# Kernel tuning notes

Hardware: AMD Instinct MI355X
Metric: run time of the kernel (lower is better)

## Reference

```python
import jax, jax.numpy as jnp
import numpy as np

B, S, E = 8, 1024, 512
H = 8            # num_heads
D = E // H       # head_dim
FFN = 2048
WINDOW = 5       # local_window_size
EPS = 1e-5


def _mha(x, in_w, in_b, out_w, out_b, mask=None):
    """PyTorch nn.MultiheadAttention (batch_first) forward. mask: True = blocked."""
    b, s, e = x.shape
    qkv = x @ in_w.T + in_b                      # [B,S,3E]
    q, k, v = jnp.split(qkv, 3, axis=-1)
    def heads(t):
        return t.reshape(b, s, H, D).transpose(0, 2, 1, 3)  # [B,H,S,D]
    q, k, v = heads(q), heads(k), heads(v)
    scores = jnp.einsum('bhsd,bhtd->bhst', q, k) / np.sqrt(D).astype(x.dtype)
    if mask is not None:
        scores = jnp.where(mask[None, None], -jnp.inf, scores)
    attn = jax.nn.softmax(scores, axis=-1)
    out = jnp.einsum('bhst,bhtd->bhsd', attn, v)  # [B,H,S,D]
    out = out.transpose(0, 2, 1, 3).reshape(b, s, e)
    return out @ out_w.T + out_b


def _layernorm(x, g, b):
    mu = jnp.mean(x, axis=-1, keepdims=True)
    var = jnp.mean(jnp.square(x - mu), axis=-1, keepdims=True)
    return (x - mu) * jax.lax.rsqrt(var + EPS) * g + b


def setup_inputs() -> dict:
    key = jax.random.key(0)
    ks = jax.random.split(key, 8)
    w = 0.02  # weight scale for numerical sanity
    return {
        'x': jax.random.normal(ks[0], (B, S, E), jnp.float32),
        'l_in_w': jax.random.normal(ks[1], (3 * E, E), jnp.float32) * w,
        'l_in_b': jnp.zeros((3 * E,), jnp.float32),
        'l_out_w': jax.random.normal(ks[2], (E, E), jnp.float32) * w,
        'l_out_b': jnp.zeros((E,), jnp.float32),
        'g_in_w': jax.random.normal(ks[3], (3 * E, E), jnp.float32) * w,
        'g_in_b': jnp.zeros((3 * E,), jnp.float32),
        'g_out_w': jax.random.normal(ks[4], (E, E), jnp.float32) * w,
        'g_out_b': jnp.zeros((E,), jnp.float32),
        'ffn_w1': jax.random.normal(ks[5], (FFN, E), jnp.float32) * w,
        'ffn_b1': jnp.zeros((FFN,), jnp.float32),
        'ffn_w2': jax.random.normal(ks[6], (E, FFN), jnp.float32) * w,
        'ffn_b2': jnp.zeros((E,), jnp.float32),
        'ln1_g': jnp.ones((E,), jnp.float32),
        'ln1_b': jnp.zeros((E,), jnp.float32),
        'ln2_g': jnp.ones((E,), jnp.float32),
        'ln2_b': jnp.zeros((E,), jnp.float32),
    }


def reference(x, l_in_w, l_in_b, l_out_w, l_out_b,
              g_in_w, g_in_b, g_out_w, g_out_b,
              ffn_w1, ffn_b1, ffn_w2, ffn_b2,
              ln1_g, ln1_b, ln2_g, ln2_b):
    s = x.shape[1]
    idx = jnp.arange(s)
    local_mask = jnp.abs(idx[:, None] - idx[None, :]) > WINDOW  # True = blocked
    local_out = _mha(x, l_in_w, l_in_b, l_out_w, l_out_b, mask=local_mask)
    global_out = _mha(x, g_in_w, g_in_b, g_out_w, g_out_b)
    x = x + local_out + global_out
    x = _layernorm(x, ln1_g, ln1_b)
    ffn = jax.nn.relu(x @ ffn_w1.T + ffn_b1) @ ffn_w2.T + ffn_b2
    x = _layernorm(x + ffn, ln2_g, ln2_b)
    return x
```

## Files before the change

kernel.cpp:

```cpp
#include <hip/hip_runtime.h>
#include <hip/hip_bf16.h>
#include <stdint.h>

#define Bb 8
#define Ss 1024
#define Ee 512
#define Hh 8
#define Dh 64
#define FFNd 2048
#define EPSv 1e-5f
#define QS 3072

typedef float f32x4 __attribute__((ext_vector_type(4)));
typedef int   i32x4 __attribute__((ext_vector_type(4)));

__device__ inline float bf2f(ushort u) {
    uint32_t x = ((uint32_t)u) << 16; float f; __builtin_memcpy(&f, &x, 4); return f;
}
__device__ inline ushort f2bf(float f) {
    uint32_t x; __builtin_memcpy(&x, &f, 4);
    uint32_t r = (x + 0x7FFFu + ((x >> 16) & 1u)) >> 16; return (ushort)r;
}

__device__ inline void gload16(const ushort* g, ushort* l) {
    __builtin_amdgcn_global_load_lds((const __attribute__((address_space(1))) void*)g,
                                     (__attribute__((address_space(3))) void*)l,
                                     16, 0, 0);
}

__device__ inline int vswz(int d, int kv) {
    return (d * 64 + kv) ^ ((((d & 7) ^ ((d >> 3) & 7)) & 7) << 3);
}

__global__ __launch_bounds__(256) void cvt_all(const float* __restrict__ s0, const float* __restrict__ s1,
                                               const float* __restrict__ s2, const float* __restrict__ s3,
                                               const float* __restrict__ s4, const float* __restrict__ s5,
                                               const float* __restrict__ s6,
                                               ushort* __restrict__ dx, ushort* __restrict__ dw) {
    int bid = blockIdx.x;
    const float* src; ushort* dst; int boff;
    if (bid < 4096)      { src = s0; dst = dx;            boff = bid; }
    else if (bid < 4864) { src = s1; dst = dw;            boff = bid - 4096; }
    else if (bid < 5632) { src = s2; dst = dw + 786432;   boff = bid - 4864; }
    else if (bid < 5888) { src = s3; dst = dw + 1572864;  boff = bid - 5632; }
    else if (bid < 6144) { src = s4; dst = dw + 1835008;  boff = bid - 5888; }
    else if (bid < 7168) { src = s5; dst = dw + 2097152;  boff = bid - 6144; }
    else                 { src = s6; dst = dw + 3145728;  boff = bid - 7168; }
    int i = boff * 256 + threadIdx.x;
    float4 v = ((const float4*)src)[i];
    ushort4 o;
    o.x = f2bf(v.x); o.y = f2bf(v.y); o.z = f2bf(v.z); o.w = f2bf(v.w);
    ((ushort4*)dst)[i] = o;
}

template<bool OUT_BF16, bool RELU>
__global__ __launch_bounds__(256) void gemm_bt(const ushort* __restrict__ A,
                                               const ushort* __restrict__ Bm,
                                               const float* __restrict__ bias,
                                               const float* __restrict__ bias2, int nb1,
                                               void* __restrict__ C,
                                               int M, int N, int K) {
    __shared__ ushort Alds[128 * 32];
    __shared__ ushort Blds[128 * 32];
    int tid  = threadIdx.x;
    int lane = tid & 63, w = tid >> 6;
    int wr = w >> 1, wc = w & 1;
    int g  = lane >> 4, fr = lane & 15;
    int m0 = blockIdx.y * 128, n0 = blockIdx.x * 128;

    int lr4 = lane >> 2;
    int lc8 = (lane & 3) * 8;
    const ushort* gA0 = A  + (size_t)(m0 + (w * 2) * 16 + lr4) * K + lc8;
    const ushort* gA1 = gA0 + (size_t)16 * K;
    const ushort* gB0 = Bm + (size_t)(n0 + (w * 2) * 16 + lr4) * K + lc8;
    const ushort* gB1 = gB0 + (size_t)16 * K;
    ushort* lA0 = Alds + (w * 2) * 16 * 32;
    ushort* lA1 = lA0 + 16 * 32;
    ushort* lB0 = Blds + (w * 2) * 16 * 32;
    ushort* lB1 = lB0 + 16 * 32;

    f32x4 acc[4][4] = {};

    for (int kb = 0; kb < K; kb += 32) {
        __syncthreads();
        gload16(gA0 + kb, lA0);
        gload16(gA1 + kb, lA1);
        gload16(gB0 + kb, lB0);
        gload16(gB1 + kb, lB1);
        __syncthreads();
        i32x4 af[4], bfr[4];
        #pragma unroll
        for (int mt = 0; mt < 4; ++mt)
            af[mt] = *(const i32x4*)(Alds + (wr * 64 + mt * 16 + fr) * 32 + g * 8);
        #pragma unroll
        for (int nt = 0; nt < 4; ++nt)
            bfr[nt] = *(const i32x4*)(Blds + (wc * 64 + nt * 16 + fr) * 32 + g * 8);
        #pragma unroll
        for (int mt = 0; mt < 4; ++mt)
            #pragma unroll
            for (int nt = 0; nt < 4; ++nt)
                asm("v_mfma_f32_16x16x32_bf16 %0, %1, %2, %0"
                    : "+v"(acc[mt][nt]) : "v"(af[mt]), "v"(bfr[nt]));
    }

    #pragma unroll
    for (int mt = 0; mt < 4; ++mt) {
        int r0 = m0 + wr * 64 + mt * 16 + g * 4;
        #pragma unroll
        for (int nt = 0; nt < 4; ++nt) {
            int c = n0 + wc * 64 + nt * 16 + fr;
            float bv = c < nb1 ? bias[c] : bias2[c - nb1];
            #pragma unroll
            for (int r = 0; r < 4; ++r) {
                float v = acc[mt][nt][r] + bv;
                if (RELU) v = v > 0.f ? v : 0.f;
                if (OUT_BF16) ((ushort*)C)[(size_t)(r0 + r) * N + c] = f2bf(v);
                else          ((float*)C)[(size_t)(r0 + r) * N + c] = v;
            }
        }
    }
}

__global__ __launch_bounds__(256) void attn_global_mfma(const ushort* __restrict__ qkv,
                                                        ushort* __restrict__ out) {
    __shared__ ushort Klds[64 * 64];
    __shared__ ushort Vtlds[64 * 64];
    __shared__ ushort Plds[4][32 * 64];
    int tid  = threadIdx.x;
    int lane = tid & 63, w = tid >> 6;
    int fr = lane & 15, g = lane >> 4;
    int qtile = blockIdx.x & 7;
    int bh = blockIdx.x >> 3;
    int h = bh & 7, b = bh >> 3;
    const ushort* qp    = qkv + (size_t)b * Ss * QS + h * Dh;
    const ushort* kbase = qp + Ee;
    const ushort* vbase = qp + 2 * Ee;

    i32x4 qf[2][2];
    int q0 = qtile * 128 + w * 32;
    #pragma unroll
    for (int mt = 0; mt < 2; ++mt)
        #pragma unroll
        for (int kb = 0; kb < 2; ++kb)
            qf[mt][kb] = *(const i32x4*)(qp + (size_t)(q0 + mt * 16 + fr) * QS + kb * 32 + g * 8);

    f32x4 oacc[2][4] = {};
    f32x4 lsum[2] = {};
    ushort* Pw = Plds[w];

    i32x4 kr[2], vr[2];
    auto load_tile = [&](int kv0) {
        #pragma unroll
        for (int u = 0; u < 2; ++u) {
            int c = tid + u * 256;
            int row = c >> 3, col8 = c & 7;
            kr[u] = *(const i32x4*)(kbase + (size_t)(kv0 + row) * QS + col8 * 8);
            vr[u] = *(const i32x4*)(vbase + (size_t)(kv0 + row) * QS + col8 * 8);
        }
    };
    load_tile(0);

    for (int kt = 0; kt < 16; ++kt) {
        __syncthreads();
        #pragma unroll
        for (int u = 0; u < 2; ++u) {
            int c = tid + u * 256;
            int row = c >> 3, col8 = c & 7;
            int kidx = (row * 64 + col8 * 8) ^ ((row & 7) << 3);
            *(i32x4*)(Klds + kidx) = kr[u];
            ushort tmp[8];
            *(i32x4*)tmp = vr[u];
            #pragma unroll
            for (int j = 0; j < 8; ++j)
                Vtlds[vswz(col8 * 8 + j, row)] = tmp[j];
        }
        __syncthreads();
        if (kt < 15) load_tile((kt + 1) * 64);

        f32x4 sacc[2][4] = {};
        i32x4 kf[4][2];
        #pragma unroll
        for (int nt = 0; nt < 4; ++nt) {
            int kvl = nt * 16 + fr;
            #pragma unroll
            for (int kb = 0; kb < 2; ++kb)
                kf[nt][kb] = *(const i32x4*)(Klds + ((kvl * 64 + kb * 32 + g * 8) ^ ((kvl & 7) << 3)));
        }
        #pragma unroll
        for (int mt = 0; mt < 2; ++mt)
            #pragma unroll
            for (int nt = 0; nt < 4; ++nt)
                #pragma unroll
                for (int kb = 0; kb < 2; ++kb)
                    asm("v_mfma_f32_16x16x32_bf16 %0, %1, %2, %0"
                        : "+v"(sacc[mt][nt]) : "v"(qf[mt][kb]), "v"(kf[nt][kb]));

        #pragma unroll
        for (int mt = 0; mt < 2; ++mt) {
            #pragma unroll
            for (int r = 0; r < 4; ++r) {
                int ql = mt * 16 + g * 4 + r;
                int sw = (ql & 7) << 3;
                float e0 = __expf(sacc[mt][0][r] * 0.125f);
                float e1 = __expf(sacc[mt][1][r] * 0.125f);
                float e2 = __expf(sacc[mt][2][r] * 0.125f);
                float e3 = __expf(sacc[mt][3][r] * 0.125f);
                Pw[(ql * 64 +  0 + fr) ^ sw] = f2bf(e0);
                Pw[(ql * 64 + 16 + fr) ^ sw] = f2bf(e1);
                Pw[(ql * 64 + 32 + fr) ^ sw] = f2bf(e2);
                Pw[(ql * 64 + 48 + fr) ^ sw] = f2bf(e3);
                lsum[mt][r] += (e0 + e1) + (e2 + e3);
            }
        }

        i32x4 pa[2][2], vf[4][2];
        #pragma unroll
        for (int mt = 0; mt < 2; ++mt) {
            int ql = mt * 16 + fr;
            #pragma unroll
            for (int kb = 0; kb < 2; ++kb)
                pa[mt][kb] = *(const i32x4*)(Pw + ((ql * 64 + kb * 32 + g * 8) ^ ((ql & 7) << 3)));
        }
        #pragma unroll
        for (int dn = 0; dn < 4; ++dn) {
            int d = dn * 16 + fr;
            #pragma unroll
            for (int kb = 0; kb < 2; ++kb)
                vf[dn][kb] = *(const i32x4*)(Vtlds + vswz(d, kb * 32 + g * 8));
        }
        #pragma unroll
        for (int mt = 0; mt < 2; ++mt)
            #pragma unroll
            for (int dn = 0; dn < 4; ++dn)
                #pragma unroll
                for (int kb = 0; kb < 2; ++kb)
                    asm("v_mfma_f32_16x16x32_bf16 %0, %1, %2, %0"
                        : "+v"(oacc[mt][dn]) : "v"(pa[mt][kb]), "v"(vf[dn][kb]));
    }

    #pragma unroll
    for (int mt = 0; mt < 2; ++mt)
        #pragma unroll
        for (int r = 0; r < 4; ++r) {
            float s = lsum[mt][r];
            s += __shfl_xor(s, 1); s += __shfl_xor(s, 2);
            s += __shfl_xor(s, 4); s += __shfl_xor(s, 8);
            lsum[mt][r] = 1.f / s;
        }

    #pragma unroll
    for (int mt = 0; mt < 2; ++mt)
        #pragma unroll
        for (int r = 0; r < 4; ++r) {
            int qg = q0 + mt * 16 + g * 4 + r;
            size_t ob = (size_t)(b * Ss + qg) * Ee + h * Dh;
            #pragma unroll
            for (int dn = 0; dn < 4; ++dn)
                out[ob + dn * 16 + fr] = f2bf(oacc[mt][dn][r] * lsum[mt][r]);
        }
}

__global__ __launch_bounds__(256) void attn_local_mfma(const ushort* __restrict__ qkv,
                                                       ushort* __restrict__ out) {
    __shared__ ushort Klds[64 * 64];
    __shared__ ushort Vtlds[64 * 64];
    __shared__ ushort Plds[4][32 * 64];
    int tid  = threadIdx.x;
    int lane = tid & 63, w = tid >> 6;
    int fr = lane & 15, g = lane >> 4;
    int qtile = blockIdx.x & 7;
    int bh = blockIdx.x >> 3;
    int h = bh & 7, b = bh >> 3;
    const ushort* qp    = qkv + (size_t)b * Ss * QS + h * Dh;
    const ushort* kbase = qp + Ee;
    const ushort* vbase = qp + 2 * Ee;

    i32x4 qf[2][2];
    int q0 = qtile * 128 + w * 32;
    #pragma unroll
    for (int mt = 0; mt < 2; ++mt)
        #pragma unroll
        for (int kb = 0; kb < 2; ++kb)
            qf[mt][kb] = *(const i32x4*)(qp + (size_t)(q0 + mt * 16 + fr) * QS + kb * 32 + g * 8);

    f32x4 oacc[2][4] = {};
    f32x4 lsum[2] = {};
    ushort* Pw = Plds[w];

    i32x4 kr[2], vr[2];
    auto load_tile = [&](int kv0) {
        #pragma unroll
        for (int u = 0; u < 2; ++u) {
            int c = tid + u * 256;
            int row = c >> 3, col8 = c & 7;
            kr[u] = *(const i32x4*)(kbase + (size_t)(kv0 + row) * QS + col8 * 8);
            vr[u] = *(const i32x4*)(vbase + (size_t)(kv0 + row) * QS + col8 * 8);
        }
    };

    int tq2 = qtile * 2;
    int kt0 = tq2 > 0 ? tq2 - 1 : 0;
    int kt1 = tq2 + 2 < 16 ? tq2 + 2 : 15;
    load_tile(kt0 * 64);

    for (int kt = kt0; kt <= kt1; ++kt) {
        int kv0 = kt * 64;
        __syncthreads();
        #pragma unroll
        for (int u = 0; u < 2; ++u) {
            int c = tid + u * 256;
            int row = c >> 3, col8 = c & 7;
            int kidx = (row * 64 + col8 * 8) ^ ((row & 7) << 3);
            *(i32x4*)(Klds + kidx) = kr[u];
            ushort tmp[8];
            *(i32x4*)tmp = vr[u];
            #pragma unroll
            for (int j = 0; j < 8; ++j)
                Vtlds[vswz(col8 * 8 + j, row)] = tmp[j];
        }
        __syncthreads();
        if (kt < kt1) load_tile((kt + 1) * 64);

        bool active = (kv0 <= q0 + 36) && (kv0 + 63 >= q0 - 5);
        if (active) {
            f32x4 sacc[2][4] = {};
            i32x4 kf[4][2];
            #pragma unroll
            for (int nt = 0; nt < 4; ++nt) {
                int kvl = nt * 16 + fr;
                #pragma unroll
                for (int kb = 0; kb < 2; ++kb)
                    kf[nt][kb] = *(const i32x4*)(Klds + ((kvl * 64 + kb * 32 + g * 8) ^ ((kvl & 7) << 3)));
            }
            #pragma unroll
            for (int mt = 0; mt < 2; ++mt)
                #pragma unroll
                for (int nt = 0; nt < 4; ++nt)
                    #pragma unroll
                    for (int kb = 0; kb < 2; ++kb)
                        asm("v_mfma_f32_16x16x32_bf16 %0, %1, %2, %0"
                            : "+v"(sacc[mt][nt]) : "v"(qf[mt][kb]), "v"(kf[nt][kb]));

            #pragma unroll
            for (int mt = 0; mt < 2; ++mt) {
                #pragma unroll
                for (int r = 0; r < 4; ++r) {
                    int ql = mt * 16 + g * 4 + r;
                    int sw = (ql & 7) << 3;
                    int d0 = (q0 + ql) - (kv0 + fr);
                    int d1 = d0 - 16, d2 = d0 - 32, d3 = d0 - 48;
                    float e0 = (d0 >= -5 && d0 <= 5) ? __expf(sacc[mt][0][r] * 0.125f) : 0.f;
                    float e1 = (d1 >= -5 && d1 <= 5) ? __expf(sacc[mt][1][r] * 0.125f) : 0.f;
                    float e2 = (d2 >= -5 && d2 <= 5) ? __expf(sacc[mt][2][r] * 0.125f) : 0.f;
                    float e3 = (d3 >= -5 && d3 <= 5) ? __expf(sacc[mt][3][r] * 0.125f) : 0.f;
                    Pw[(ql * 64 +  0 + fr) ^ sw] = f2bf(e0);
                    Pw[(ql * 64 + 16 + fr) ^ sw] = f2bf(e1);
                    Pw[(ql * 64 + 32 + fr) ^ sw] = f2bf(e2);
                    Pw[(ql * 64 + 48 + fr) ^ sw] = f2bf(e3);
                    lsum[mt][r] += (e0 + e1) + (e2 + e3);
                }
            }

            i32x4 pa[2][2], vf[4][2];
            #pragma unroll
            for (int mt = 0; mt < 2; ++mt) {
                int ql = mt * 16 + fr;
                #pragma unroll
                for (int kb = 0; kb < 2; ++kb)
                    pa[mt][kb] = *(const i32x4*)(Pw + ((ql * 64 + kb * 32 + g * 8) ^ ((ql & 7) << 3)));
            }
            #pragma unroll
            for (int dn = 0; dn < 4; ++dn) {
                int d = dn * 16 + fr;
                #pragma unroll
                for (int kb = 0; kb < 2; ++kb)
                    vf[dn][kb] = *(const i32x4*)(Vtlds + vswz(d, kb * 32 + g * 8));
            }
            #pragma unroll
            for (int mt = 0; mt < 2; ++mt)
                #pragma unroll
                for (int dn = 0; dn < 4; ++dn)
                    #pragma unroll
                    for (int kb = 0; kb < 2; ++kb)
                        asm("v_mfma_f32_16x16x32_bf16 %0, %1, %2, %0"
                            : "+v"(oacc[mt][dn]) : "v"(pa[mt][kb]), "v"(vf[dn][kb]));
        }
    }

    #pragma unroll
    for (int mt = 0; mt < 2; ++mt)
        #pragma unroll
        for (int r = 0; r < 4; ++r) {
            float s = lsum[mt][r];
            s += __shfl_xor(s, 1); s += __shfl_xor(s, 2);
            s += __shfl_xor(s, 4); s += __shfl_xor(s, 8);
            lsum[mt][r] = 1.f / s;
        }

    #pragma unroll
    for (int mt = 0; mt < 2; ++mt)
        #pragma unroll
        for (int r = 0; r < 4; ++r) {
            int qg = q0 + mt * 16 + g * 4 + r;
            size_t ob = (size_t)(b * Ss + qg) * Ee + h * Dh;
            #pragma unroll
            for (int dn = 0; dn < 4; ++dn)
                out[ob + dn * 16 + fr] = f2bf(oacc[mt][dn][r] * lsum[mt][r]);
        }
}

__global__ __launch_bounds__(256) void ln_add3(const float* __restrict__ x,
                                               const float* __restrict__ p1,
                                               const float* __restrict__ p2,
                                               const float* __restrict__ gam,
                                               const float* __restrict__ bet,
                                               ushort* __restrict__ yb,
                                               float* __restrict__ yf) {
    int row  = blockIdx.x * 4 + (threadIdx.x >> 6);
    int lane = threadIdx.x & 63;
    size_t off = (size_t)row * Ee + lane * 8;
    float hv[8];
    float4 a0 = *(const float4*)(x + off),  a1 = *(const float4*)(x + off + 4);
    float4 b0 = *(const float4*)(p1 + off), b1 = *(const float4*)(p1 + off + 4);
    float4 c0 = *(const float4*)(p2 + off), c1 = *(const float4*)(p2 + off + 4);
    hv[0] = a0.x + b0.x + c0.x; hv[1] = a0.y + b0.y + c0.y;
    hv[2] = a0.z + b0.z + c0.z; hv[3] = a0.w + b0.w + c0.w;
    hv[4] = a1.x + b1.x + c1.x; hv[5] = a1.y + b1.y + c1.y;
    hv[6] = a1.z + b1.z + c1.z; hv[7] = a1.w + b1.w + c1.w;
    float s = 0.f;
    #pragma unroll
    for (int i = 0; i < 8; ++i) s += hv[i];
    #pragma unroll
    for (int o = 32; o; o >>= 1) s += __shfl_xor(s, o);
    float mu = s * (1.f / Ee);
    float vs = 0.f;
    #pragma unroll
    for (int i = 0; i < 8; ++i) { float d = hv[i] - mu; vs += d * d; }
    #pragma unroll
    for (int o = 32; o; o >>= 1) vs += __shfl_xor(vs, o);
    float rs = rsqrtf(vs * (1.f / Ee) + EPSv);
    #pragma unroll
    for (int i = 0; i < 8; ++i) {
        float yv = (hv[i] - mu) * rs * gam[lane * 8 + i] + bet[lane * 8 + i];
        yf[off + i] = yv;
        yb[off + i] = f2bf(yv);
    }
}

__global__ __launch_bounds__(256) void ln_add2(const float* __restrict__ a,
                                               const float* __restrict__ bsrc,
                                               const float* __restrict__ gam,
                                               const float* __restrict__ bet,
                                               float* __restrict__ outp) {
    int row  = blockIdx.x * 4 + (threadIdx.x >> 6);
    int lane = threadIdx.x & 63;
    size_t off = (size_t)row * Ee + lane * 8;
    float hv[8];
    float4 a0 = *(const float4*)(a + off),    a1 = *(const float4*)(a + off + 4);
    float4 b0 = *(const float4*)(bsrc + off), b1 = *(const float4*)(bsrc + off + 4);
    hv[0] = a0.x + b0.x; hv[1] = a0.y + b0.y; hv[2] = a0.z + b0.z; hv[3] = a0.w + b0.w;
    hv[4] = a1.x + b1.x; hv[5] = a1.y + b1.y; hv[6] = a1.z + b1.z; hv[7] = a1.w + b1.w;
    float s = 0.f;
    #pragma unroll
    for (int i = 0; i < 8; ++i) s += hv[i];
    #pragma unroll
    for (int o = 32; o; o >>= 1) s += __shfl_xor(s, o);
    float mu = s * (1.f / Ee);
    float vs = 0.f;
    #pragma unroll
    for (int i = 0; i < 8; ++i) { float d = hv[i] - mu; vs += d * d; }
    #pragma unroll
    for (int o = 32; o; o >>= 1) vs += __shfl_xor(vs, o);
    float rs = rsqrtf(vs * (1.f / Ee) + EPSv);
    #pragma unroll
    for (int i = 0; i < 8; ++i)
        outp[off + i] = (hv[i] - mu) * rs * gam[lane * 8 + i] + bet[lane * 8 + i];
}

extern "C" void kernel_launch(void* const* d_in, const int* in_sizes, int n_in,
                              void* d_out, int out_size, void* d_ws, size_t ws_size,
                              hipStream_t stream) {
    const float* x      = (const float*)d_in[0];
    const float* l_in_w = (const float*)d_in[1];
    const float* l_in_b = (const float*)d_in[2];
    const float* l_out_w= (const float*)d_in[3];
    const float* l_out_b= (const float*)d_in[4];
    const float* g_in_w = (const float*)d_in[5];
    const float* g_in_b = (const float*)d_in[6];
    const float* g_out_w= (const float*)d_in[7];
    const float* g_out_b= (const float*)d_in[8];
    const float* ffn_w1 = (const float*)d_in[9];
    const float* ffn_b1 = (const float*)d_in[10];
    const float* ffn_w2 = (const float*)d_in[11];
    const float* ffn_b2 = (const float*)d_in[12];
    const float* ln1_g  = (const float*)d_in[13];
    const float* ln1_b  = (const float*)d_in[14];
    const float* ln2_g  = (const float*)d_in[15];
    const float* ln2_b  = (const float*)d_in[16];

    char* ws = (char*)d_ws;
    ushort* xb       = (ushort*)(ws + 0);
    ushort* wb       = (ushort*)(ws + 8388608);
    ushort* l_out_wb = wb + 1572864;
    ushort* w1b      = wb + 2097152;
    ushort* w2b      = wb + 3145728;
    ushort* g_out_wb = wb + 1835008;
    ushort* qkvb     = (ushort*)(ws + 16777216);
    ushort* attnLb   = (ushort*)(ws + 67108864);
    ushort* attnGb   = (ushort*)(ws + 75497472);
    float*  projL    = (float*)(ws + 16777216);
    float*  projG    = (float*)(ws + 33554432);
    ushort* y1b      = (ushort*)(ws + 50331648);
    float*  y1f      = (float*)(ws + 58720256);
    ushort* ffn1b    = (ushort*)(ws + 16777216);
    float*  ffn2f    = (float*)(ws + 75497472);

    const int M = Bb * Ss;

    cvt_all<<<dim3(8192), dim3(256), 0, stream>>>(x, l_in_w, g_in_w, l_out_w, g_out_w,
                                                  ffn_w1, ffn_w2, xb, wb);

    gemm_bt<true, false><<<dim3(24, 64), 256, 0, stream>>>(
        xb, wb, l_in_b, g_in_b, 1536, qkvb, M, QS, Ee);

    attn_local_mfma<<<dim3(Bb * Hh * (Ss / 128)), 256, 0, stream>>>(qkvb, attnLb);
    attn_global_mfma<<<dim3(Bb * Hh * (Ss / 128)), 256, 0, stream>>>(qkvb + 1536, attnGb);

    gemm_bt<false, false><<<dim3(4, 64), 256, 0, stream>>>(
        attnLb, l_out_wb, l_out_b, l_out_b, Ee, projL, M, Ee, Ee);
    gemm_bt<false, false><<<dim3(4, 64), 256, 0, stream>>>(
        attnGb, g_out_wb, g_out_b, g_out_b, Ee, projG, M, Ee, Ee);

    ln_add3<<<dim3(M / 4), 256, 0, stream>>>(x, projL, projG, ln1_g, ln1_b, y1b, y1f);

    gemm_bt<true, true><<<dim3(16, 64), 256, 0, stream>>>(
        y1b, w1b, ffn_b1, ffn_b1, FFNd, ffn1b, M, FFNd, Ee);
    gemm_bt<false, false><<<dim3(4, 64), 256, 0, stream>>>(
        ffn1b, w2b, ffn_b2, ffn_b2, Ee, ffn2f, M, Ee, FFNd);

    ln_add2<<<dim3(M / 4), 256, 0, stream>>>(y1f, ffn2f, ln2_g, ln2_b, (float*)d_out);
}
```

Baseline: 319.0 us.

## Merge local and global output projections into one K=1024 GEMM

The local and global attention outputs are written side by side into one concatenated [M,1024] buffer, and the two out-projection weights are interleaved into one [512,1024] matrix during conversion. A single GEMM with summed biases then replaces the two separate projection GEMMs and the extra fp32 intermediate, so the LayerNorm reads two inputs instead of three. A new 64x128-tile GEMM kernel is used for the N=512 projections, including FFN2, to raise the block count for these narrow outputs, at the cost of less reuse per tile.

```diff
diff --git a/kernel.cpp b/kernel.cpp
--- a/kernel.cpp
+++ b/kernel.cpp
@@ -10,6 +10,7 @@
 #define FFNd 2048
 #define EPSv 1e-5f
 #define QS 3072
+#define OS 1024
 
 typedef float f32x4 __attribute__((ext_vector_type(4)));
 typedef int   i32x4 __attribute__((ext_vector_type(4)));
@@ -32,25 +33,27 @@
     return (d * 64 + kv) ^ ((((d & 7) ^ ((d >> 3) & 7)) & 7) << 3);
 }
 
+__device__ inline void cvt4_to(const float* src, int f, ushort* dst) {
+    float4 v = *(const float4*)(src + f);
+    ushort4 o;
+    o.x = f2bf(v.x); o.y = f2bf(v.y); o.z = f2bf(v.z); o.w = f2bf(v.w);
+    *(ushort4*)dst = o;
+}
 __global__ __launch_bounds__(256) void cvt_all(const float* __restrict__ s0, const float* __restrict__ s1,
                                                const float* __restrict__ s2, const float* __restrict__ s3,
                                                const float* __restrict__ s4, const float* __restrict__ s5,
                                                const float* __restrict__ s6,
                                                ushort* __restrict__ dx, ushort* __restrict__ dw) {
-    int bid = blockIdx.x;
-    const float* src; ushort* dst; int boff;
-    if (bid < 4096)      { src = s0; dst = dx;            boff = bid; }
-    else if (bid < 4864) { src = s1; dst = dw;            boff = bid - 4096; }
-    else if (bid < 5632) { src = s2; dst = dw + 786432;   boff = bid - 4864; }
-    else if (bid < 5888) { src = s3; dst = dw + 1572864;  boff = bid - 5632; }
-    else if (bid < 6144) { src = s4; dst = dw + 1835008;  boff = bid - 5888; }
-    else if (bid < 7168) { src = s5; dst = dw + 2097152;  boff = bid - 6144; }
-    else                 { src = s6; dst = dw + 3145728;  boff = bid - 7168; }
-    int i = boff * 256 + threadIdx.x;
-    float4 v = ((const float4*)src)[i];
-    ushort4 o;
-    o.x = f2bf(v.x); o.y = f2bf(v.y); o.z = f2bf(v.z); o.w = f2bf(v.w);
-    ((ushort4*)dst)[i] = o;
+    int bid = blockIdx.x, tid = threadIdx.x;
+    if (bid < 4096)      { int f = bid * 1024 + tid * 4;          cvt4_to(s0, f, dx + f); }
+    else if (bid < 4864) { int f = (bid - 4096) * 1024 + tid * 4; cvt4_to(s1, f, dw + f); }
+    else if (bid < 5632) { int f = (bid - 4864) * 1024 + tid * 4; cvt4_to(s2, f, dw + 786432 + f); }
+    else if (bid < 5888) { int f = (bid - 5632) * 1024 + tid * 4; int n = f >> 9, k = f & 511;
+                           cvt4_to(s3, f, dw + 1572864 + n * 1024 + k); }
+    else if (bid < 6144) { int f = (bid - 5888) * 1024 + tid * 4; int n = f >> 9, k = f & 511;
+                           cvt4_to(s4, f, dw + 1572864 + n * 1024 + 512 + k); }
+    else if (bid < 7168) { int f = (bid - 6144) * 1024 + tid * 4; cvt4_to(s5, f, dw + 2097152 + f); }
+    else                 { int f = (bid - 7168) * 1024 + tid * 4; cvt4_to(s6, f, dw + 3145728 + f); }
 }
 
 template<bool OUT_BF16, bool RELU>
@@ -121,6 +124,66 @@
     }
 }
 
+template<bool SUMB>
+__global__ __launch_bounds__(256) void gemm64(const ushort* __restrict__ A,
+                                              const ushort* __restrict__ Bm,
+                                              const float* __restrict__ bias,
+                                              const float* __restrict__ bias2,
+                                              float* __restrict__ C,
+                                              int M, int N, int K) {
+    __shared__ ushort Alds[64 * 32];
+    __shared__ ushort Blds[128 * 32];
+    int tid  = threadIdx.x;
+    int lane = tid & 63, w = tid >> 6;
+    int g  = lane >> 4, fr = lane & 15;
+    int m0 = blockIdx.y * 64, n0 = blockIdx.x * 128;
+
+    int lr4 = lane >> 2;
+    int lc8 = (lane & 3) * 8;
+    const ushort* gA  = A  + (size_t)(m0 + w * 16 + lr4) * K + lc8;
+    const ushort* gB0 = Bm + (size_t)(n0 + w * 32 + lr4) * K + lc8;
+    const ushort* gB1 = gB0 + (size_t)16 * K;
+    ushort* lA  = Alds + w * 16 * 32;
+    ushort* lB0 = Blds + w * 32 * 32;
+    ushort* lB1 = lB0 + 16 * 32;
+
+    f32x4 acc[4][2] = {};
+
+    for (int kb = 0; kb < K; kb += 32) {
+        __syncthreads();
+        gload16(gA + kb, lA);
+        gload16(gB0 + kb, lB0);
+        gload16(gB1 + kb, lB1);
+        __syncthreads();
+        i32x4 af[4], bfr[2];
+        #pragma unroll
+        for (int mt = 0; mt < 4; ++mt)
+            af[mt] = *(const i32x4*)(Alds + (mt * 16 + fr) * 32 + g * 8);
+        #pragma unroll
+        for (int nt = 0; nt < 2; ++nt)
+            bfr[nt] = *(const i32x4*)(Blds + (w * 32 + nt * 16 + fr) * 32 + g * 8);
+        #pragma unroll
+        for (int mt = 0; mt < 4; ++mt)
+            #pragma unroll
+            for (int nt = 0; nt < 2; ++nt)
+                asm("v_mfma_f32_16x16x32_bf16 %0, %1, %2, %0"
+                    : "+v"(acc[mt][nt]) : "v"(af[mt]), "v"(bfr[nt]));
+    }
+
+    #pragma unroll
+    for (int mt = 0; mt < 4; ++mt) {
+        int r0 = m0 + mt * 16 + g * 4;
+        #pragma unroll
+        for (int nt = 0; nt < 2; ++nt) {
+            int c = n0 + w * 32 + nt * 16 + fr;
+            float bv = SUMB ? bias[c] + bias2[c] : bias[c];
+            #pragma unroll
+            for (int r = 0; r < 4; ++r)
+                C[(size_t)(r0 + r) * N + c] = acc[mt][nt][r] + bv;
+        }
+    }
+}
+
 __global__ __launch_bounds__(256) void attn_global_mfma(const ushort* __restrict__ qkv,
                                                         ushort* __restrict__ out) {
     __shared__ ushort Klds[64 * 64];
@@ -253,7 +316,7 @@
         #pragma unroll
         for (int r = 0; r < 4; ++r) {
             int qg = q0 + mt * 16 + g * 4 + r;
-            size_t ob = (size_t)(b * Ss + qg) * Ee + h * Dh;
+            size_t ob = (size_t)(b * Ss + qg) * OS + h * Dh;
             #pragma unroll
             for (int dn = 0; dn < 4; ++dn)
                 out[ob + dn * 16 + fr] = f2bf(oacc[mt][dn][r] * lsum[mt][r]);
@@ -402,31 +465,27 @@
         #pragma unroll
         for (int r = 0; r < 4; ++r) {
             int qg = q0 + mt * 16 + g * 4 + r;
-            size_t ob = (size_t)(b * Ss + qg) * Ee + h * Dh;
+            size_t ob = (size_t)(b * Ss + qg) * OS + h * Dh;
             #pragma unroll
             for (int dn = 0; dn < 4; ++dn)
                 out[ob + dn * 16 + fr] = f2bf(oacc[mt][dn][r] * lsum[mt][r]);
         }
 }
 
-__global__ __launch_bounds__(256) void ln_add3(const float* __restrict__ x,
-                                               const float* __restrict__ p1,
-                                               const float* __restrict__ p2,
-                                               const float* __restrict__ gam,
-                                               const float* __restrict__ bet,
-                                               ushort* __restrict__ yb,
-                                               float* __restrict__ yf) {
+__global__ __launch_bounds__(256) void ln_add2_dw(const float* __restrict__ x,
+                                                  const float* __restrict__ p1,
+                                                  const float* __restrict__ gam,
+                                                  const float* __restrict__ bet,
+                                                  ushort* __restrict__ yb,
+                                                  float* __restrict__ yf) {
     int row  = blockIdx.x * 4 + (threadIdx.x >> 6);
     int lane = threadIdx.x & 63;
     size_t off = (size_t)row * Ee + lane * 8;
     float hv[8];
     float4 a0 = *(const float4*)(x + off),  a1 = *(const float4*)(x + off + 4);
     float4 b0 = *(const float4*)(p1 + off), b1 = *(const float4*)(p1 + off + 4);
-    float4 c0 = *(const float4*)(p2 + off), c1 = *(const float4*)(p2 + off + 4);
-    hv[0] = a0.x + b0.x + c0.x; hv[1] = a0.y + b0.y + c0.y;
-    hv[2] = a0.z + b0.z + c0.z; hv[3] = a0.w + b0.w + c0.w;
-    hv[4] = a1.x + b1.x + c1.x; hv[5] = a1.y + b1.y + c1.y;
-    hv[6] = a1.z + b1.z + c1.z; hv[7] = a1.w + b1.w + c1.w;
+    hv[0] = a0.x + b0.x; hv[1] = a0.y + b0.y; hv[2] = a0.z + b0.z; hv[3] = a0.w + b0.w;
+    hv[4] = a1.x + b1.x; hv[5] = a1.y + b1.y; hv[6] = a1.z + b1.z; hv[7] = a1.w + b1.w;
     float s = 0.f;
     #pragma unroll
     for (int i = 0; i < 8; ++i) s += hv[i];
@@ -501,15 +560,12 @@
     char* ws = (char*)d_ws;
     ushort* xb       = (ushort*)(ws + 0);
     ushort* wb       = (ushort*)(ws + 8388608);
-    ushort* l_out_wb = wb + 1572864;
+    ushort* w_cat    = wb + 1572864;
     ushort* w1b      = wb + 2097152;
     ushort* w2b      = wb + 3145728;
-    ushort* g_out_wb = wb + 1835008;
     ushort* qkvb     = (ushort*)(ws + 16777216);
-    ushort* attnLb   = (ushort*)(ws + 67108864);
-    ushort* attnGb   = (ushort*)(ws + 75497472);
-    float*  projL    = (float*)(ws + 16777216);
-    float*  projG    = (float*)(ws + 33554432);
+    ushort* attnCat  = (ushort*)(ws + 67108864);
+    float*  projM    = (float*)(ws + 16777216);
     ushort* y1b      = (ushort*)(ws + 50331648);
     float*  y1f      = (float*)(ws + 58720256);
     ushort* ffn1b    = (ushort*)(ws + 16777216);
@@ -523,20 +579,18 @@
     gemm_bt<true, false><<<dim3(24, 64), 256, 0, stream>>>(
         xb, wb, l_in_b, g_in_b, 1536, qkvb, M, QS, Ee);
 
-    attn_local_mfma<<<dim3(Bb * Hh * (Ss / 128)), 256, 0, stream>>>(qkvb, attnLb);
-    attn_global_mfma<<<dim3(Bb * Hh * (Ss / 128)), 256, 0, stream>>>(qkvb + 1536, attnGb);
-
-    gemm_bt<false, false><<<dim3(4, 64), 256, 0, stream>>>(
-        attnLb, l_out_wb, l_out_b, l_out_b, Ee, projL, M, Ee, Ee);
-    gemm_bt<false, false><<<dim3(4, 64), 256, 0, stream>>>(
-        attnGb, g_out_wb, g_out_b, g_out_b, Ee, projG, M, Ee, Ee);
-
-    ln_add3<<<dim3(M / 4), 256, 0, stream>>>(x, projL, projG, ln1_g, ln1_b, y1b, y1f);
+    attn_local_mfma<<<dim3(Bb * Hh * (Ss / 128)), 256, 0, stream>>>(qkvb, attnCat);
+    attn_global_mfma<<<dim3(Bb * Hh * (Ss / 128)), 256, 0, stream>>>(qkvb + 1536, attnCat + 512);
+
+    gemm64<true><<<dim3(Ee / 128, M / 64), 256, 0, stream>>>(
+        attnCat, w_cat, l_out_b, g_out_b, projM, M, Ee, 1024);
+
+    ln_add2_dw<<<dim3(M / 4), 256, 0, stream>>>(x, projM, ln1_g, ln1_b, y1b, y1f);
 
     gemm_bt<true, true><<<dim3(16, 64), 256, 0, stream>>>(
         y1b, w1b, ffn_b1, ffn_b1, FFNd, ffn1b, M, FFNd, Ee);
-    gemm_bt<false, false><<<dim3(4, 64), 256, 0, stream>>>(
-        ffn1b, w2b, ffn_b2, ffn_b2, Ee, ffn2f, M, Ee, FFNd);
+    gemm64<false><<<dim3(Ee / 128, M / 64), 256, 0, stream>>>(
+        ffn1b, w2b, ffn_b2, ffn_b2, ffn2f, M, Ee, FFNd);
 
     ln_add2<<<dim3(M / 4), 256, 0, stream>>>(y1f, ffn2f, ln2_g, ln2_b, (float*)d_out);
 }
```

Result: faster. 296.6 us (-7.0%).
